# Kernel tuning notes

Measured on AMD Instinct MI355X. Metric: run time of the kernel, lower is better.

## Reference

```python
import jax, jax.numpy as jnp
import numpy as np


def setup_inputs() -> dict:
    key = jax.random.key(0)
    k1, k2, k3 = jax.random.split(key, 3)
    B, S, H, KVH, D = 2, 2048, 32, 8, 128
    NUM_SLOTS = 8192  # paged KV cache capacity (token slots)
    xq = jax.random.normal(k1, (B, S, H, D), dtype=jnp.float32)
    xk = jax.random.normal(k2, (B, S, KVH, D), dtype=jnp.float32)
    xv = jax.random.normal(k3, (B, S, KVH, D), dtype=jnp.float32)
    kv_buffer = jnp.zeros((NUM_SLOTS, 2 * KVH, D), dtype=jnp.float32)
    select_index = jnp.arange(B * S, dtype=jnp.int64 if jax.config.jax_enable_x64 else jnp.int32)
    return {"xq": xq, "xk": xk, "xv": xv, "kv_buffer": kv_buffer, "select_index": select_index}


def reference(xq, xk, xv, kv_buffer, select_index):
    # context_forward (prefill): scatter K/V into the paged cache, then
    # causal GQA flash-attention over the new sequence.
    B, S, H, D = xq.shape
    KVH = xk.shape[2]
    G = H // KVH  # query heads per kv head

    # --- paged KV-cache append (scatter write by flat token slot) ---
    flat_k = xk.reshape(B * S, KVH, D)
    flat_v = xv.reshape(B * S, KVH, D)
    kv_new = kv_buffer.at[select_index, :KVH, :].set(flat_k)
    kv_new = kv_new.at[select_index, KVH:, :].set(flat_v)

    # --- causal attention (flash_attention_v2 math) ---
    scale = 1.0 / jnp.sqrt(jnp.asarray(D, dtype=xq.dtype))
    qr = xq.reshape(B, S, KVH, G, D)
    # scores: [B, KVH, G, Sq, Sk]
    scores = jnp.einsum("bqhgd,bkhd->bhgqk", qr, xk) * scale
    causal = jnp.tril(jnp.ones((S, S), dtype=bool))
    scores = jnp.where(causal, scores, jnp.finfo(scores.dtype).min)
    p = jax.nn.softmax(scores, axis=-1)
    out = jnp.einsum("bhgqk,bkhd->bqhgd", p, xv).reshape(B, S, H * D)
    return out, kv_new
```

## Files before the change

### kernel.cpp

```cpp
#include <hip/hip_runtime.h>

typedef __attribute__((ext_vector_type(8))) __bf16 bf16x8;
typedef __attribute__((ext_vector_type(8))) unsigned short ushort8;
typedef __attribute__((ext_vector_type(4))) unsigned short us4;
typedef __attribute__((ext_vector_type(4))) float f32x4;
typedef __attribute__((ext_vector_type(4))) float f4;

union BF8 { ushort8 u; bf16x8 b; };

#define NB 2
#define NS 2048
#define NH 32
#define NKVH 8
#define ND 128
#define QBLK 64
#define KVBLK 32
#define QK_SCALE 0.08838834764831845f
#define SM_SHIFT 12.0f

__device__ __forceinline__ unsigned short f2bf(float f) {
  unsigned u = __float_as_uint(f);
  return (unsigned short)((u + 0x7FFFu + ((u >> 16) & 1u)) >> 16);
}

__global__ __launch_bounds__(256) void attn_fwd(
    const float* __restrict__ xq, const float* __restrict__ xk,
    const float* __restrict__ xv, float* __restrict__ out) {
  __shared__ unsigned short K_lds[KVBLK * ND];
  __shared__ unsigned short VT_lds[ND * KVBLK];
  __shared__ unsigned short P_lds[4 * 16 * 40];

  const int qt = (int)gridDim.x - 1 - (int)blockIdx.x;
  const int h = blockIdx.y;
  const int b = blockIdx.z;
  const int kvh = h >> 2;
  const int q0 = qt * QBLK;
  const int tid = threadIdx.x;
  const int wid = tid >> 6;
  const int lane = tid & 63;
  const int m16 = lane & 15;
  const int g = lane >> 4;
  const int wq0 = q0 + wid * 16;

  BF8 qf[4];
  {
    const float* qrow = xq + ((size_t)((b * NS + wq0 + m16) * NH + h)) * ND;
#pragma unroll
    for (int c = 0; c < 4; ++c) {
      const float* src = qrow + c * 32 + g * 8;
      f4 a = *(const f4*)src;
      f4 bb = *(const f4*)(src + 4);
      ushort8 u;
      u[0] = f2bf(a[0] * QK_SCALE);  u[1] = f2bf(a[1] * QK_SCALE);
      u[2] = f2bf(a[2] * QK_SCALE);  u[3] = f2bf(a[3] * QK_SCALE);
      u[4] = f2bf(bb[0] * QK_SCALE); u[5] = f2bf(bb[1] * QK_SCALE);
      u[6] = f2bf(bb[2] * QK_SCALE); u[7] = f2bf(bb[3] * QK_SCALE);
      qf[c].u = u;
    }
  }

  f32x4 acc[8];
#pragma unroll
  for (int i = 0; i < 8; ++i) acc[i] = f32x4{0.f, 0.f, 0.f, 0.f};
  float l_r[4] = {0.f, 0.f, 0.f, 0.f};

  const int kr = tid >> 3;
  const int kc0 = (tid & 7) * 16;
  const int vcb = tid & 31;
  const int vr4 = tid >> 5;
  const int ksw = (kr & 7) << 4;
  const char* vbase = (const char*)VT_lds + m16 * 64 + ((g ^ (m16 >> 2)) << 4);

  const int nt = (q0 + QBLK) / KVBLK;
  for (int it = 0; it < nt; ++it) {
    const int k0 = it * KVBLK;
    __syncthreads();
    {
      const float* ks = xk + ((size_t)((b * NS + k0 + kr) * NKVH + kvh)) * ND + kc0;
      f4 a0 = *(const f4*)ks;       f4 a1 = *(const f4*)(ks + 4);
      f4 a2 = *(const f4*)(ks + 8); f4 a3 = *(const f4*)(ks + 12);
      ushort8 w0, w1;
      w0[0]=f2bf(a0[0]); w0[1]=f2bf(a0[1]); w0[2]=f2bf(a0[2]); w0[3]=f2bf(a0[3]);
      w0[4]=f2bf(a1[0]); w0[5]=f2bf(a1[1]); w0[6]=f2bf(a1[2]); w0[7]=f2bf(a1[3]);
      w1[0]=f2bf(a2[0]); w1[1]=f2bf(a2[1]); w1[2]=f2bf(a2[2]); w1[3]=f2bf(a2[3]);
      w1[4]=f2bf(a3[0]); w1[5]=f2bf(a3[1]); w1[6]=f2bf(a3[2]); w1[7]=f2bf(a3[3]);
      char* kbase = (char*)K_lds + kr * 256;
      *(ushort8*)(kbase + ((kc0 * 2) ^ ksw)) = w0;
      *(ushort8*)(kbase + ((kc0 * 2 + 16) ^ ksw)) = w1;

      const float* vs = xv + ((size_t)((b * NS + k0 + 4 * vr4) * NKVH + kvh)) * ND + 4 * vcb;
      f4 v0 = *(const f4*)vs;
      f4 v1 = *(const f4*)(vs + NKVH * ND);
      f4 v2 = *(const f4*)(vs + 2 * NKVH * ND);
      f4 v3 = *(const f4*)(vs + 3 * NKVH * ND);
      char* vwb = (char*)VT_lds + (vr4 & 1) * 8;
      const int vch = vr4 >> 1;
#pragma unroll
      for (int i = 0; i < 4; ++i) {
        const int d = 4 * vcb + i;
        us4 w;
        w[0] = f2bf(v0[i]); w[1] = f2bf(v1[i]); w[2] = f2bf(v2[i]); w[3] = f2bf(v3[i]);
        *(us4*)(vwb + d * 64 + ((vch ^ (vcb & 3)) << 4)) = w;
      }
    }
    __syncthreads();

    const bool active_w = (k0 <= wq0 + 15);
    if (active_w) {
      f32x4 s0 = f32x4{0.f,0.f,0.f,0.f}, s1 = f32x4{0.f,0.f,0.f,0.f};
#pragma unroll
      for (int c = 0; c < 4; ++c) {
        const int cb = 64 * c + 16 * g;
        BF8 kf0, kf1;
        kf0.u = *(const ushort8*)((const char*)K_lds + m16 * 256 + (cb ^ ((m16 & 7) << 4)));
        kf1.u = *(const ushort8*)((const char*)K_lds + (m16 + 16) * 256 + (cb ^ ((m16 & 7) << 4)));
        s0 = __builtin_amdgcn_mfma_f32_16x16x32_bf16(qf[c].b, kf0.b, s0, 0, 0, 0);
        s1 = __builtin_amdgcn_mfma_f32_16x16x32_bf16(qf[c].b, kf1.b, s1, 0, 0, 0);
      }
      if (k0 + KVBLK - 1 > wq0) {
#pragma unroll
        for (int j = 0; j < 4; ++j) {
          const int qj = wq0 + 4 * g + j;
          if (k0 + m16 > qj)      s0[j] = -1e30f;
          if (k0 + 16 + m16 > qj) s1[j] = -1e30f;
        }
      }
      float p0v[4], p1v[4];
#pragma unroll
      for (int j = 0; j < 4; ++j) {
        p0v[j] = __expf(s0[j] - SM_SHIFT);
        p1v[j] = __expf(s1[j] - SM_SHIFT);
        l_r[j] += p0v[j] + p1v[j];
      }
      unsigned short* pw = P_lds + wid * (16 * 40);
#pragma unroll
      for (int j = 0; j < 4; ++j) {
        pw[(4 * g + j) * 40 + m16]      = f2bf(p0v[j]);
        pw[(4 * g + j) * 40 + m16 + 16] = f2bf(p1v[j]);
      }
      asm volatile("s_waitcnt lgkmcnt(0)" ::: "memory");
      __builtin_amdgcn_sched_barrier(0);
      BF8 pa;
      pa.u = *(const ushort8*)(pw + m16 * 40 + g * 8);
#pragma unroll
      for (int ot = 0; ot < 8; ++ot) {
        BF8 vb;
        vb.u = *(const ushort8*)(vbase + ot * 1024);
        acc[ot] = __builtin_amdgcn_mfma_f32_16x16x32_bf16(pa.b, vb.b, acc[ot], 0, 0, 0);
      }
    }
  }

#pragma unroll
  for (int off = 1; off < 16; off <<= 1) {
#pragma unroll
    for (int j = 0; j < 4; ++j) l_r[j] += __shfl_xor(l_r[j], off);
  }
  float inv[4];
#pragma unroll
  for (int j = 0; j < 4; ++j) inv[j] = 1.0f / l_r[j];
#pragma unroll
  for (int ot = 0; ot < 8; ++ot) {
#pragma unroll
    for (int j = 0; j < 4; ++j) {
      const int q = wq0 + 4 * g + j;
      out[(size_t)(b * NS + q) * (NH * ND) + h * ND + ot * 16 + m16] = acc[ot][j] * inv[j];
    }
  }
}

__global__ void kv_copy(const f4* __restrict__ src, f4* __restrict__ dst, int n4) {
  int i = blockIdx.x * blockDim.x + threadIdx.x;
  const int stride = gridDim.x * blockDim.x;
  for (; i < n4; i += stride) dst[i] = src[i];
}

__global__ void kv_scatter(const f4* __restrict__ xk, const f4* __restrict__ xv,
                           const int* __restrict__ sel, f4* __restrict__ dst) {
  const int tok = blockIdx.x;
  const int j = threadIdx.x;
  const int slot = sel[tok];
  dst[(size_t)slot * 512 + j]       = xk[(size_t)tok * 256 + j];
  dst[(size_t)slot * 512 + 256 + j] = xv[(size_t)tok * 256 + j];
}

extern "C" void kernel_launch(void* const* d_in, const int* in_sizes, int n_in,
                              void* d_out, int out_size, void* d_ws, size_t ws_size,
                              hipStream_t stream) {
  const float* xq = (const float*)d_in[0];
  const float* xk = (const float*)d_in[1];
  const float* xv = (const float*)d_in[2];
  const float* kvbuf = (const float*)d_in[3];
  const int* sel = (const int*)d_in[4];
  float* out = (float*)d_out;
  float* out_kv = out + (size_t)NB * NS * NH * ND;

  dim3 grid(NS / QBLK, NH, NB);
  attn_fwd<<<grid, 256, 0, stream>>>(xq, xk, xv, out);

  kv_copy<<<2048, 256, 0, stream>>>((const f4*)kvbuf, (f4*)out_kv,
                                    (8192 * 16 * 128) / 4);
  kv_scatter<<<NB * NS, 256, 0, stream>>>((const f4*)xk, (const f4*)xv, sel, (f4*)out_kv);
}
```

Baseline: 564.1 us.

## Pre-convert K/V to swizzled bf16 tiles, double-buffer via global_load_lds, 128-row Q blocks

Adds two pre-pass kernels that convert K and V to bf16 once, writing K in its LDS-swizzled tile layout and V transposed into a workspace. The attention kernel then streams these tiles directly into double-buffered LDS with global_load_lds, prefetching the next tile during compute. Each block also handles 128 query rows, two 16-row slices per wave, so every loaded K/V tile is reused for twice as many queries. This removes the conversion and transpose work that every head and query block repeated, and overlaps loads with MFMA. The cost is extra launches, workspace traffic, more registers per thread and half as many blocks.

```diff
diff --git a/kernel.cpp b/kernel.cpp
--- a/kernel.cpp
+++ b/kernel.cpp
@@ -2,7 +2,6 @@
 
 typedef __attribute__((ext_vector_type(8))) __bf16 bf16x8;
 typedef __attribute__((ext_vector_type(8))) unsigned short ushort8;
-typedef __attribute__((ext_vector_type(4))) unsigned short us4;
 typedef __attribute__((ext_vector_type(4))) float f32x4;
 typedef __attribute__((ext_vector_type(4))) float f4;
 
@@ -13,158 +12,236 @@
 #define NH 32
 #define NKVH 8
 #define ND 128
-#define QBLK 64
+#define QBLK 128
 #define KVBLK 32
+#define NT (NS / KVBLK)
+#define KTILE_SH 4096
 #define QK_SCALE 0.08838834764831845f
 #define SM_SHIFT 12.0f
+
+#define GLOAD16(gp, lp) __builtin_amdgcn_global_load_lds( \
+    (const __attribute__((address_space(1))) unsigned int*)(gp), \
+    (__attribute__((address_space(3))) unsigned int*)(lp), 16, 0, 0)
 
 __device__ __forceinline__ unsigned short f2bf(float f) {
   unsigned u = __float_as_uint(f);
   return (unsigned short)((u + 0x7FFFu + ((u >> 16) & 1u)) >> 16);
 }
 
+__global__ __launch_bounds__(256) void conv_k(const float* __restrict__ xk,
+                                              unsigned short* __restrict__ Kg) {
+  const int idx = blockIdx.x * 256 + threadIdx.x;
+  const int c   = idx & 15;
+  const int r   = (idx >> 4) & 31;
+  const int s   = ((idx >> 9) & 63) * 32 + r;
+  const int kvh = (idx >> 15) & 7;
+  const int b   = idx >> 18;
+  const float* src = xk + ((size_t)((b * NS + s) * NKVH + kvh)) * ND + ((c ^ (r & 7)) * 8);
+  f4 a = *(const f4*)src;
+  f4 q = *(const f4*)(src + 4);
+  ushort8 w;
+  w[0]=f2bf(a[0]); w[1]=f2bf(a[1]); w[2]=f2bf(a[2]); w[3]=f2bf(a[3]);
+  w[4]=f2bf(q[0]); w[5]=f2bf(q[1]); w[6]=f2bf(q[2]); w[7]=f2bf(q[3]);
+  *(ushort8*)(Kg + (size_t)idx * 8) = w;
+}
+
+__global__ __launch_bounds__(256) void conv_vt(const float* __restrict__ xv,
+                                               unsigned short* __restrict__ Vg) {
+  const int idx = blockIdx.x * 256 + threadIdx.x;
+  const int cc  = idx & 3;
+  const int d   = (idx >> 2) & 127;
+  const int t   = (idx >> 9) & 63;
+  const int kvh = (idx >> 15) & 7;
+  const int b   = idx >> 18;
+  const int kv0 = t * 32 + ((cc ^ ((d >> 2) & 3)) << 3);
+  const float* src = xv + ((size_t)((b * NS + kv0) * NKVH + kvh)) * ND + d;
+  ushort8 w;
+#pragma unroll
+  for (int i = 0; i < 8; ++i) w[i] = f2bf(src[(size_t)i * (NKVH * ND)]);
+  *(ushort8*)(Vg + (size_t)idx * 8) = w;
+}
+
 __global__ __launch_bounds__(256) void attn_fwd(
-    const float* __restrict__ xq, const float* __restrict__ xk,
-    const float* __restrict__ xv, float* __restrict__ out) {
-  __shared__ unsigned short K_lds[KVBLK * ND];
-  __shared__ unsigned short VT_lds[ND * KVBLK];
-  __shared__ unsigned short P_lds[4 * 16 * 40];
+    const float* __restrict__ xq, const unsigned short* __restrict__ Kg,
+    const unsigned short* __restrict__ Vg, float* __restrict__ out) {
+  __shared__ unsigned short Kb[2][KTILE_SH];
+  __shared__ unsigned short Vb[2][KTILE_SH];
+  __shared__ unsigned short P_lds[2][4][640];
 
   const int qt = (int)gridDim.x - 1 - (int)blockIdx.x;
-  const int h = blockIdx.y;
-  const int b = blockIdx.z;
+  const int h = blockIdx.y, b = blockIdx.z;
   const int kvh = h >> 2;
   const int q0 = qt * QBLK;
-  const int tid = threadIdx.x;
-  const int wid = tid >> 6;
-  const int lane = tid & 63;
-  const int m16 = lane & 15;
-  const int g = lane >> 4;
-  const int wq0 = q0 + wid * 16;
-
-  BF8 qf[4];
+  const int tid = threadIdx.x, wid = tid >> 6, lane = tid & 63;
+  const int m16 = lane & 15, g = lane >> 4;
+  const int wqA = q0 + wid * 16, wqB = wqA + 64;
+
+  BF8 qfA[4], qfB[4];
   {
-    const float* qrow = xq + ((size_t)((b * NS + wq0 + m16) * NH + h)) * ND;
+    const float* qa = xq + ((size_t)((b * NS + wqA + m16) * NH + h)) * ND;
+    const float* qb = xq + ((size_t)((b * NS + wqB + m16) * NH + h)) * ND;
 #pragma unroll
     for (int c = 0; c < 4; ++c) {
-      const float* src = qrow + c * 32 + g * 8;
-      f4 a = *(const f4*)src;
-      f4 bb = *(const f4*)(src + 4);
-      ushort8 u;
-      u[0] = f2bf(a[0] * QK_SCALE);  u[1] = f2bf(a[1] * QK_SCALE);
-      u[2] = f2bf(a[2] * QK_SCALE);  u[3] = f2bf(a[3] * QK_SCALE);
-      u[4] = f2bf(bb[0] * QK_SCALE); u[5] = f2bf(bb[1] * QK_SCALE);
-      u[6] = f2bf(bb[2] * QK_SCALE); u[7] = f2bf(bb[3] * QK_SCALE);
-      qf[c].u = u;
-    }
-  }
-
-  f32x4 acc[8];
-#pragma unroll
-  for (int i = 0; i < 8; ++i) acc[i] = f32x4{0.f, 0.f, 0.f, 0.f};
-  float l_r[4] = {0.f, 0.f, 0.f, 0.f};
-
-  const int kr = tid >> 3;
-  const int kc0 = (tid & 7) * 16;
-  const int vcb = tid & 31;
-  const int vr4 = tid >> 5;
-  const int ksw = (kr & 7) << 4;
-  const char* vbase = (const char*)VT_lds + m16 * 64 + ((g ^ (m16 >> 2)) << 4);
+      const float* sa = qa + c * 32 + g * 8;
+      const float* sb = qb + c * 32 + g * 8;
+      f4 a0 = *(const f4*)sa; f4 a1 = *(const f4*)(sa + 4);
+      f4 b0 = *(const f4*)sb; f4 b1 = *(const f4*)(sb + 4);
+      ushort8 ua, ub;
+#pragma unroll
+      for (int j = 0; j < 4; ++j) {
+        ua[j] = f2bf(a0[j] * QK_SCALE); ua[j + 4] = f2bf(a1[j] * QK_SCALE);
+        ub[j] = f2bf(b0[j] * QK_SCALE); ub[j + 4] = f2bf(b1[j] * QK_SCALE);
+      }
+      qfA[c].u = ua; qfB[c].u = ub;
+    }
+  }
+
+  f32x4 accA[8], accB[8];
+#pragma unroll
+  for (int i = 0; i < 8; ++i) {
+    accA[i] = f32x4{0.f, 0.f, 0.f, 0.f};
+    accB[i] = f32x4{0.f, 0.f, 0.f, 0.f};
+  }
+  float lA[4] = {0.f, 0.f, 0.f, 0.f}, lB[4] = {0.f, 0.f, 0.f, 0.f};
+
+  const size_t panel = ((size_t)(b * NKVH + kvh)) * NT * KTILE_SH;
+  const unsigned short* Kp = Kg + panel;
+  const unsigned short* Vp = Vg + panel;
+  const int o0 = wid * 2048, o1 = o0 + 1024;
+  const int lo = lane * 16;
+  const int vboff = m16 * 64 + ((g ^ (m16 >> 2)) << 4);
+  const int kswz = (m16 & 7) << 4;
 
   const int nt = (q0 + QBLK) / KVBLK;
+  {
+    const char* kt = (const char*)(Kp);
+    const char* vt = (const char*)(Vp);
+    GLOAD16(kt + o0 + lo, (char*)Kb[0] + o0);
+    GLOAD16(kt + o1 + lo, (char*)Kb[0] + o1);
+    GLOAD16(vt + o0 + lo, (char*)Vb[0] + o0);
+    GLOAD16(vt + o1 + lo, (char*)Vb[0] + o1);
+  }
+  int cur = 0;
   for (int it = 0; it < nt; ++it) {
+    __syncthreads();
+    if (it + 1 < nt) {
+      const char* kt = (const char*)(Kp + (size_t)(it + 1) * KTILE_SH);
+      const char* vt = (const char*)(Vp + (size_t)(it + 1) * KTILE_SH);
+      GLOAD16(kt + o0 + lo, (char*)Kb[cur ^ 1] + o0);
+      GLOAD16(kt + o1 + lo, (char*)Kb[cur ^ 1] + o1);
+      GLOAD16(vt + o0 + lo, (char*)Vb[cur ^ 1] + o0);
+      GLOAD16(vt + o1 + lo, (char*)Vb[cur ^ 1] + o1);
+    }
     const int k0 = it * KVBLK;
-    __syncthreads();
-    {
-      const float* ks = xk + ((size_t)((b * NS + k0 + kr) * NKVH + kvh)) * ND + kc0;
-      f4 a0 = *(const f4*)ks;       f4 a1 = *(const f4*)(ks + 4);
-      f4 a2 = *(const f4*)(ks + 8); f4 a3 = *(const f4*)(ks + 12);
-      ushort8 w0, w1;
-      w0[0]=f2bf(a0[0]); w0[1]=f2bf(a0[1]); w0[2]=f2bf(a0[2]); w0[3]=f2bf(a0[3]);
-      w0[4]=f2bf(a1[0]); w0[5]=f2bf(a1[1]); w0[6]=f2bf(a1[2]); w0[7]=f2bf(a1[3]);
-      w1[0]=f2bf(a2[0]); w1[1]=f2bf(a2[1]); w1[2]=f2bf(a2[2]); w1[3]=f2bf(a2[3]);
-      w1[4]=f2bf(a3[0]); w1[5]=f2bf(a3[1]); w1[6]=f2bf(a3[2]); w1[7]=f2bf(a3[3]);
-      char* kbase = (char*)K_lds + kr * 256;
-      *(ushort8*)(kbase + ((kc0 * 2) ^ ksw)) = w0;
-      *(ushort8*)(kbase + ((kc0 * 2 + 16) ^ ksw)) = w1;
-
-      const float* vs = xv + ((size_t)((b * NS + k0 + 4 * vr4) * NKVH + kvh)) * ND + 4 * vcb;
-      f4 v0 = *(const f4*)vs;
-      f4 v1 = *(const f4*)(vs + NKVH * ND);
-      f4 v2 = *(const f4*)(vs + 2 * NKVH * ND);
-      f4 v3 = *(const f4*)(vs + 3 * NKVH * ND);
-      char* vwb = (char*)VT_lds + (vr4 & 1) * 8;
-      const int vch = vr4 >> 1;
-#pragma unroll
-      for (int i = 0; i < 4; ++i) {
-        const int d = 4 * vcb + i;
-        us4 w;
-        w[0] = f2bf(v0[i]); w[1] = f2bf(v1[i]); w[2] = f2bf(v2[i]); w[3] = f2bf(v3[i]);
-        *(us4*)(vwb + d * 64 + ((vch ^ (vcb & 3)) << 4)) = w;
-      }
-    }
-    __syncthreads();
-
-    const bool active_w = (k0 <= wq0 + 15);
-    if (active_w) {
-      f32x4 s0 = f32x4{0.f,0.f,0.f,0.f}, s1 = f32x4{0.f,0.f,0.f,0.f};
-#pragma unroll
-      for (int c = 0; c < 4; ++c) {
-        const int cb = 64 * c + 16 * g;
-        BF8 kf0, kf1;
-        kf0.u = *(const ushort8*)((const char*)K_lds + m16 * 256 + (cb ^ ((m16 & 7) << 4)));
-        kf1.u = *(const ushort8*)((const char*)K_lds + (m16 + 16) * 256 + (cb ^ ((m16 & 7) << 4)));
-        s0 = __builtin_amdgcn_mfma_f32_16x16x32_bf16(qf[c].b, kf0.b, s0, 0, 0, 0);
-        s1 = __builtin_amdgcn_mfma_f32_16x16x32_bf16(qf[c].b, kf1.b, s1, 0, 0, 0);
-      }
-      if (k0 + KVBLK - 1 > wq0) {
+    const bool aB = (k0 <= wqB + 15);
+    const bool aA = (k0 <= wqA + 15);
+    if (aB) {
+      const char* kb = (const char*)Kb[cur];
+      f32x4 sA0 = f32x4{0.f,0.f,0.f,0.f}, sA1 = f32x4{0.f,0.f,0.f,0.f};
+      f32x4 sB0 = f32x4{0.f,0.f,0.f,0.f}, sB1 = f32x4{0.f,0.f,0.f,0.f};
+      if (aA) {
+#pragma unroll
+        for (int c = 0; c < 4; ++c) {
+          const int cb = 64 * c + 16 * g;
+          BF8 kf0, kf1;
+          kf0.u = *(const ushort8*)(kb + m16 * 256 + (cb ^ kswz));
+          kf1.u = *(const ushort8*)(kb + (m16 + 16) * 256 + (cb ^ kswz));
+          sB0 = __builtin_amdgcn_mfma_f32_16x16x32_bf16(qfB[c].b, kf0.b, sB0, 0, 0, 0);
+          sB1 = __builtin_amdgcn_mfma_f32_16x16x32_bf16(qfB[c].b, kf1.b, sB1, 0, 0, 0);
+          sA0 = __builtin_amdgcn_mfma_f32_16x16x32_bf16(qfA[c].b, kf0.b, sA0, 0, 0, 0);
+          sA1 = __builtin_amdgcn_mfma_f32_16x16x32_bf16(qfA[c].b, kf1.b, sA1, 0, 0, 0);
+        }
+      } else {
+#pragma unroll
+        for (int c = 0; c < 4; ++c) {
+          const int cb = 64 * c + 16 * g;
+          BF8 kf0, kf1;
+          kf0.u = *(const ushort8*)(kb + m16 * 256 + (cb ^ kswz));
+          kf1.u = *(const ushort8*)(kb + (m16 + 16) * 256 + (cb ^ kswz));
+          sB0 = __builtin_amdgcn_mfma_f32_16x16x32_bf16(qfB[c].b, kf0.b, sB0, 0, 0, 0);
+          sB1 = __builtin_amdgcn_mfma_f32_16x16x32_bf16(qfB[c].b, kf1.b, sB1, 0, 0, 0);
+        }
+      }
+      if (k0 + KVBLK - 1 > wqB) {
 #pragma unroll
         for (int j = 0; j < 4; ++j) {
-          const int qj = wq0 + 4 * g + j;
-          if (k0 + m16 > qj)      s0[j] = -1e30f;
-          if (k0 + 16 + m16 > qj) s1[j] = -1e30f;
-        }
-      }
-      float p0v[4], p1v[4];
-#pragma unroll
-      for (int j = 0; j < 4; ++j) {
-        p0v[j] = __expf(s0[j] - SM_SHIFT);
-        p1v[j] = __expf(s1[j] - SM_SHIFT);
-        l_r[j] += p0v[j] + p1v[j];
-      }
-      unsigned short* pw = P_lds + wid * (16 * 40);
-#pragma unroll
-      for (int j = 0; j < 4; ++j) {
-        pw[(4 * g + j) * 40 + m16]      = f2bf(p0v[j]);
-        pw[(4 * g + j) * 40 + m16 + 16] = f2bf(p1v[j]);
+          const int qj = wqB + 4 * g + j;
+          if (k0 + m16 > qj)      sB0[j] = -1e30f;
+          if (k0 + 16 + m16 > qj) sB1[j] = -1e30f;
+        }
+      }
+      {
+        unsigned short* pw = &P_lds[1][wid][0];
+#pragma unroll
+        for (int j = 0; j < 4; ++j) {
+          const float p0 = __expf(sB0[j] - SM_SHIFT);
+          const float p1 = __expf(sB1[j] - SM_SHIFT);
+          lB[j] += p0 + p1;
+          pw[(4 * g + j) * 40 + m16]      = f2bf(p0);
+          pw[(4 * g + j) * 40 + m16 + 16] = f2bf(p1);
+        }
+      }
+      if (aA) {
+        if (k0 + KVBLK - 1 > wqA) {
+#pragma unroll
+          for (int j = 0; j < 4; ++j) {
+            const int qj = wqA + 4 * g + j;
+            if (k0 + m16 > qj)      sA0[j] = -1e30f;
+            if (k0 + 16 + m16 > qj) sA1[j] = -1e30f;
+          }
+        }
+        unsigned short* pw = &P_lds[0][wid][0];
+#pragma unroll
+        for (int j = 0; j < 4; ++j) {
+          const float p0 = __expf(sA0[j] - SM_SHIFT);
+          const float p1 = __expf(sA1[j] - SM_SHIFT);
+          lA[j] += p0 + p1;
+          pw[(4 * g + j) * 40 + m16]      = f2bf(p0);
+          pw[(4 * g + j) * 40 + m16 + 16] = f2bf(p1);
+        }
       }
       asm volatile("s_waitcnt lgkmcnt(0)" ::: "memory");
       __builtin_amdgcn_sched_barrier(0);
-      BF8 pa;
-      pa.u = *(const ushort8*)(pw + m16 * 40 + g * 8);
-#pragma unroll
-      for (int ot = 0; ot < 8; ++ot) {
-        BF8 vb;
-        vb.u = *(const ushort8*)(vbase + ot * 1024);
-        acc[ot] = __builtin_amdgcn_mfma_f32_16x16x32_bf16(pa.b, vb.b, acc[ot], 0, 0, 0);
-      }
-    }
+      const char* vb0 = (const char*)Vb[cur] + vboff;
+      BF8 paB; paB.u = *(const ushort8*)(&P_lds[1][wid][0] + m16 * 40 + g * 8);
+      if (aA) {
+        BF8 paA; paA.u = *(const ushort8*)(&P_lds[0][wid][0] + m16 * 40 + g * 8);
+#pragma unroll
+        for (int ot = 0; ot < 8; ++ot) {
+          BF8 vf; vf.u = *(const ushort8*)(vb0 + ot * 1024);
+          accB[ot] = __builtin_amdgcn_mfma_f32_16x16x32_bf16(paB.b, vf.b, accB[ot], 0, 0, 0);
+          accA[ot] = __builtin_amdgcn_mfma_f32_16x16x32_bf16(paA.b, vf.b, accA[ot], 0, 0, 0);
+        }
+      } else {
+#pragma unroll
+        for (int ot = 0; ot < 8; ++ot) {
+          BF8 vf; vf.u = *(const ushort8*)(vb0 + ot * 1024);
+          accB[ot] = __builtin_amdgcn_mfma_f32_16x16x32_bf16(paB.b, vf.b, accB[ot], 0, 0, 0);
+        }
+      }
+    }
+    cur ^= 1;
   }
 
 #pragma unroll
   for (int off = 1; off < 16; off <<= 1) {
 #pragma unroll
-    for (int j = 0; j < 4; ++j) l_r[j] += __shfl_xor(l_r[j], off);
-  }
-  float inv[4];
-#pragma unroll
-  for (int j = 0; j < 4; ++j) inv[j] = 1.0f / l_r[j];
+    for (int j = 0; j < 4; ++j) {
+      lA[j] += __shfl_xor(lA[j], off);
+      lB[j] += __shfl_xor(lB[j], off);
+    }
+  }
+  float invA[4], invB[4];
+#pragma unroll
+  for (int j = 0; j < 4; ++j) { invA[j] = 1.0f / lA[j]; invB[j] = 1.0f / lB[j]; }
 #pragma unroll
   for (int ot = 0; ot < 8; ++ot) {
 #pragma unroll
     for (int j = 0; j < 4; ++j) {
-      const int q = wq0 + 4 * g + j;
-      out[(size_t)(b * NS + q) * (NH * ND) + h * ND + ot * 16 + m16] = acc[ot][j] * inv[j];
+      const int qA = wqA + 4 * g + j;
+      const int qB = wqB + 4 * g + j;
+      out[(size_t)(b * NS + qA) * (NH * ND) + h * ND + ot * 16 + m16] = accA[ot][j] * invA[j];
+      out[(size_t)(b * NS + qB) * (NH * ND) + h * ND + ot * 16 + m16] = accB[ot][j] * invB[j];
     }
   }
 }
@@ -195,8 +272,14 @@
   float* out = (float*)d_out;
   float* out_kv = out + (size_t)NB * NS * NH * ND;
 
+  unsigned short* Kg = (unsigned short*)d_ws;
+  unsigned short* Vg = Kg + (size_t)NB * NKVH * NT * KTILE_SH;
+
+  conv_k <<<2048, 256, 0, stream>>>(xk, Kg);
+  conv_vt<<<2048, 256, 0, stream>>>(xv, Vg);
+
   dim3 grid(NS / QBLK, NH, NB);
-  attn_fwd<<<grid, 256, 0, stream>>>(xq, xk, xv, out);
+  attn_fwd<<<grid, 256, 0, stream>>>(xq, Kg, Vg, out);
 
   kv_copy<<<2048, 256, 0, stream>>>((const f4*)kvbuf, (f4*)out_kv,
                                     (8192 * 16 * 128) / 4);
```

Measured after the change: 484.0 us. -14.2%, faster.
